# Kernel optimization log

Hardware: AMD Instinct MI355X
Metric: run time of the kernel (lower is better)

Reference implementation:

```python
import jax, jax.numpy as jnp
import numpy as np

N = 50000       # nodes
E = 1_600_000   # edges (before self-loops)
IN = 128        # in_channels
OUT = 32        # out_channels per head
H = 2           # heads
NEG_SLOPE = 0.2 # PyG GATConv default leaky-relu slope


def setup_inputs() -> dict:
    key = jax.random.key(0)
    k = jax.random.split(key, 6)
    x = jax.random.normal(k[0], (N, IN), jnp.float32)
    edge_index = jax.random.randint(k[1], (2, E), 0, N, dtype=jnp.int64)
    W = jax.random.normal(k[2], (IN, H * OUT), jnp.float32) / np.sqrt(IN).astype(np.float32)
    att_src = jax.random.normal(k[3], (H, OUT), jnp.float32) * 0.1
    att_dst = jax.random.normal(k[4], (H, OUT), jnp.float32) * 0.1
    bias = jax.random.normal(k[5], (H * OUT,), jnp.float32) * 0.01
    return {"x": x, "edge_index": edge_index, "W": W,
            "att_src": att_src, "att_dst": att_dst, "bias": bias}


def reference(x, edge_index, W, att_src, att_dst, bias):
    n = x.shape[0]
    h_, c = att_src.shape
    # add self-loops (PyG GATConv default add_self_loops=True)
    loops = jnp.arange(n, dtype=edge_index.dtype)
    src = jnp.concatenate([edge_index[0], loops])  # [E+N]
    dst = jnp.concatenate([edge_index[1], loops])  # [E+N]
    # linear transform -> [N, H, C]
    h = (x @ W).reshape(n, h_, c)
    # per-node attention logits per head
    a_src = jnp.einsum('nhc,hc->nh', h, att_src)  # [N, H]
    a_dst = jnp.einsum('nhc,hc->nh', h, att_dst)  # [N, H]
    # per-edge scores
    e = jax.nn.leaky_relu(a_src[src] + a_dst[dst], NEG_SLOPE)  # [E+N, H]
    # segment softmax over incoming edges of each dst node
    seg_max = jax.ops.segment_max(e, dst, num_segments=n)      # [N, H]
    ex = jnp.exp(e - seg_max[dst])
    denom = jax.ops.segment_sum(ex, dst, num_segments=n)       # [N, H]
    alpha = ex / denom[dst]                                    # [E+N, H]
    # weighted scatter-aggregate of source features
    msg = alpha[:, :, None] * h[src]                           # [E+N, H, C]
    out = jax.ops.segment_sum(msg, dst, num_segments=n)        # [N, H, C]
    return out.reshape(n, h_ * c) + bias
```

## Files before the change

kernel.cpp:

```cpp
#include <hip/hip_runtime.h>
#include <hip/hip_fp16.h>

#define N_NODES 50000
#define N_EDGES 1600000
#define IN_CH   128
#define NEG     0.2f
#define NBUK    391
#define BCAP    4608
#define CAP     80
#define CHUNK   4096
#define P_BLOCKS 391
#define PT      512

__global__ __launch_bounds__(256) void gemm_logits(
    const float* __restrict__ x, const float* __restrict__ W,
    const float* __restrict__ att_src, const float* __restrict__ att_dst,
    unsigned int* __restrict__ hI, float* __restrict__ as_, float* __restrict__ ad_,
    int* __restrict__ gcur)
{
    if (blockIdx.x == 0) {
        for (int i = threadIdx.x; i < NBUK; i += 256) gcur[i] = 0;
    }

    __shared__ float Wl[IN_CH * 64];
    for (int i = threadIdx.x; i < IN_CH * 64; i += 256) Wl[i] = W[i];
    __syncthreads();

    int gid = blockIdx.x * 256 + threadIdx.x;
    int row = gid >> 2;
    int sub = gid & 3;
    if (row >= N_NODES) return;

    float acc[16];
#pragma unroll
    for (int c = 0; c < 16; ++c) acc[c] = 0.f;

    const float* xr = x + (size_t)row * IN_CH;
    for (int k = 0; k < IN_CH; k += 4) {
        float4 xv = *(const float4*)(xr + k);
        float xs[4] = {xv.x, xv.y, xv.z, xv.w};
#pragma unroll
        for (int kk = 0; kk < 4; ++kk) {
            const float* wr = &Wl[(k + kk) * 64 + sub * 16];
#pragma unroll
            for (int c = 0; c < 16; c += 4) {
                float4 wv = *(const float4*)(wr + c);
                acc[c]     += xs[kk] * wv.x;
                acc[c + 1] += xs[kk] * wv.y;
                acc[c + 2] += xs[kk] * wv.z;
                acc[c + 3] += xs[kk] * wv.w;
            }
        }
    }

    float part[16];
#pragma unroll
    for (int i = 0; i < 16; ++i) part[i] = __shfl_xor(acc[i], 2);

    if (sub < 2) {
        union { unsigned int u[16]; uint4 v4[4]; } pk;
#pragma unroll
        for (int i = 0; i < 16; ++i) {
            pk.u[i] = (unsigned)__half_as_ushort(__float2half_rn(acc[i])) |
                      ((unsigned)__half_as_ushort(__float2half_rn(part[i])) << 16);
        }
        uint4* hp = (uint4*)(hI + (size_t)row * 32 + sub * 16);
#pragma unroll
        for (int i = 0; i < 4; ++i) hp[i] = pk.v4[i];
    }

    float s = 0.f, d = 0.f;
#pragma unroll
    for (int c = 0; c < 16; ++c) {
        s += acc[c] * att_src[sub * 16 + c];
        d += acc[c] * att_dst[sub * 16 + c];
    }
    s += __shfl_xor(s, 1);
    d += __shfl_xor(d, 1);
    if ((sub & 1) == 0) {
        as_[row * 2 + (sub >> 1)] = s;
        ad_[row * 2 + (sub >> 1)] = d;
    }
}

__global__ __launch_bounds__(PT) void partition(
    const int* __restrict__ ei, int* __restrict__ gcur,
    unsigned int* __restrict__ barr)
{
    __shared__ int hist[NBUK];
    __shared__ int start[NBUK];
    __shared__ int gbase[NBUK];
    __shared__ int lofs[NBUK];
    __shared__ int wsum[8];
    __shared__ int woff[8];
    __shared__ unsigned int buf[CHUNK];

    int tid = threadIdx.x;
    int lane = tid & 63, wid = tid >> 6;
    int cbase = blockIdx.x * CHUNK;
    int cnt = N_EDGES - cbase;
    if (cnt > CHUNK) cnt = CHUNK;
    int n4 = cnt >> 2;

    for (int i = tid; i < NBUK; i += PT) { hist[i] = 0; lofs[i] = 0; }
    __syncthreads();

    const int4* s4 = (const int4*)ei + (cbase >> 2);
    const int4* d4 = (const int4*)(ei + N_EDGES) + (cbase >> 2);

    int4 dv[2], sv[2];
#pragma unroll
    for (int i = 0; i < 2; ++i) {
        int k = i * PT + tid;
        if (k < n4) {
            dv[i] = d4[k]; sv[i] = s4[k];
            atomicAdd(&hist[dv[i].x >> 7], 1);
            atomicAdd(&hist[dv[i].y >> 7], 1);
            atomicAdd(&hist[dv[i].z >> 7], 1);
            atomicAdd(&hist[dv[i].w >> 7], 1);
        }
    }
    __syncthreads();

    int a = (tid < NBUK) ? hist[tid] : 0;
    int orig = a;
#pragma unroll
    for (int off = 1; off < 64; off <<= 1) {
        int u = __shfl_up(a, off);
        if (lane >= off) a += u;
    }
    if (lane == 63) wsum[wid] = a;
    __syncthreads();
    if (tid == 0) {
        int r = 0;
#pragma unroll
        for (int w = 0; w < 8; ++w) { woff[w] = r; r += wsum[w]; }
    }
    __syncthreads();
    a += woff[wid];
    if (tid < NBUK) {
        start[tid] = a - orig;
        gbase[tid] = atomicAdd(&gcur[tid], orig);
    }
    __syncthreads();

#pragma unroll
    for (int i = 0; i < 2; ++i) {
        int k = i * PT + tid;
        if (k < n4) {
            int dd[4] = {dv[i].x, dv[i].y, dv[i].z, dv[i].w};
            int ss[4] = {sv[i].x, sv[i].y, sv[i].z, sv[i].w};
#pragma unroll
            for (int e = 0; e < 4; ++e) {
                int d = dd[e];
                int bkt = d >> 7;
                int loc = atomicAdd(&lofs[bkt], 1);
                buf[start[bkt] + loc] =
                    (unsigned)ss[e] | ((unsigned)(d & 127) << 16) | ((unsigned)bkt << 23);
            }
        }
    }
    __syncthreads();

    for (int i = tid; i < cnt; i += PT) {
        unsigned u = buf[i];
        int bkt = u >> 23;
        int g = gbase[bkt] + (i - start[bkt]);
        if (g < BCAP) barr[(size_t)bkt * BCAP + g] = u & 0x7FFFFFu;
    }
}

__global__ __launch_bounds__(1024) void aggregate(
    const unsigned int* __restrict__ hI, const float* __restrict__ as_,
    const float* __restrict__ ad_, const int* __restrict__ gcur,
    const unsigned int* __restrict__ barr, const float* __restrict__ bias,
    float* __restrict__ out)
{
    __shared__ unsigned short lcol[128 * CAP];
    __shared__ int hist[128];
    __shared__ int lofs[128];
    __shared__ int wtot;

    int b = blockIdx.x, tid = threadIdx.x;
    if (tid < 128) { hist[tid] = 0; lofs[tid] = 0; }
    __syncthreads();

    int cnt = gcur[b];
    if (cnt > BCAP) cnt = BCAP;
    const unsigned int* bb = barr + (size_t)b * BCAP;

    for (int i = tid; i < cnt; i += 1024)
        atomicAdd(&hist[(bb[i] >> 16) & 127], 1);
    __syncthreads();

    for (int i = tid; i < cnt; i += 1024) {
        unsigned u = bb[i];
        int dl = (u >> 16) & 127;
        int k = atomicAdd(&lofs[dl], 1);
        if (k < CAP) lcol[dl * CAP + k] = (unsigned short)(u & 0xFFFFu);
    }
    __syncthreads();

    int lane = tid & 63;
    int wave = tid >> 6;
    int c    = lane & 31;
    int hv   = lane >> 5;
    int sl   = lane & 32;
    float bi0 = bias[c], bi1 = bias[32 + c];

    for (int pass = 0; pass < 4; ++pass) {
        int dl = pass * 32 + (wave << 1) + hv;
        int node = b * 128 + dl;
        bool valid = (node < N_NODES);

        float2 adv = valid ? *(const float2*)(ad_ + node * 2) : make_float2(0.f, 0.f);
        float2 asv = valid ? *(const float2*)(as_ + node * 2) : make_float2(0.f, 0.f);

        float t0 = asv.x + adv.x, t1 = asv.y + adv.y;
        float e0 = (t0 > 0.f) ? t0 : NEG * t0;
        float e1 = (t1 > 0.f) ? t1 : NEG * t1;
        float p0s = __expf(e0), p1s = __expf(e1);
        unsigned hs = valid ? hI[(unsigned)node * 32u + c] : 0u;
        float h0s = __half2float(__ushort_as_half((unsigned short)(hs & 0xFFFFu)));
        float h1s = __half2float(__ushort_as_half((unsigned short)(hs >> 16)));
        float acc0a = p0s * h0s, acc0b = 0.f;
        float acc1a = p1s * h1s, acc1b = 0.f;
        float s0 = 0.f, s1 = 0.f;

        int n = valid ? min(hist[dl], CAP) : 0;
        const unsigned short* cb = &lcol[dl * CAP];
        int nmax = max(n, __shfl_xor(n, 32));

        for (int base = 0; base < nmax; base += 32) {
            unsigned pack1 = 0, pack2 = 0;
            int myidx = base + c;
            if (myidx < n) {
                int msrc = (int)cb[myidx];
                float2 av = *(const float2*)(as_ + msrc * 2);
                float u0 = av.x + adv.x, u1 = av.y + adv.y;
                float f0 = (u0 > 0.f) ? u0 : NEG * u0;
                float f1 = (u1 > 0.f) ? u1 : NEG * u1;
                float q0 = __expf(f0), q1 = __expf(f1);
                s0 += q0; s1 += q1;
                pack1 = ((unsigned)msrc << 16) |
                        (unsigned)__half_as_ushort(__float2half_rn(q0));
                pack2 = (unsigned)__half_as_ushort(__float2half_rn(q1));
            }
            int c32 = nmax - base;
            if (c32 > 32) c32 = 32;

            int jj = 0;
            for (; jj + 4 <= c32; jj += 4) {
                unsigned aA = __shfl(pack1, sl + jj);
                unsigned bA = __shfl(pack2, sl + jj);
                unsigned aB = __shfl(pack1, sl + jj + 1);
                unsigned bB = __shfl(pack2, sl + jj + 1);
                unsigned aC = __shfl(pack1, sl + jj + 2);
                unsigned bC = __shfl(pack2, sl + jj + 2);
                unsigned aD = __shfl(pack1, sl + jj + 3);
                unsigned bD = __shfl(pack2, sl + jj + 3);
                unsigned vA = hI[(aA >> 16) * 32u + c];
                unsigned vB = hI[(aB >> 16) * 32u + c];
                unsigned vC = hI[(aC >> 16) * 32u + c];
                unsigned vD = hI[(aD >> 16) * 32u + c];
                float pA0 = __half2float(__ushort_as_half((unsigned short)aA));
                float pA1 = __half2float(__ushort_as_half((unsigned short)bA));
                float pB0 = __half2float(__ushort_as_half((unsigned short)aB));
                float pB1 = __half2float(__ushort_as_half((unsigned short)bB));
                float pC0 = __half2float(__ushort_as_half((unsigned short)aC));
                float pC1 = __half2float(__ushort_as_half((unsigned short)bC));
                float pD0 = __half2float(__ushort_as_half((unsigned short)aD));
                float pD1 = __half2float(__ushort_as_half((unsigned short)bD));
                acc0a = fmaf(pA0, __half2float(__ushort_as_half((unsigned short)(vA & 0xFFFFu))), acc0a);
                acc1a = fmaf(pA1, __half2float(__ushort_as_half((unsigned short)(vA >> 16))), acc1a);
                acc0b = fmaf(pB0, __half2float(__ushort_as_half((unsigned short)(vB & 0xFFFFu))), acc0b);
                acc1b = fmaf(pB1, __half2float(__ushort_as_half((unsigned short)(vB >> 16))), acc1b);
                acc0a = fmaf(pC0, __half2float(__ushort_as_half((unsigned short)(vC & 0xFFFFu))), acc0a);
                acc1a = fmaf(pC1, __half2float(__ushort_as_half((unsigned short)(vC >> 16))), acc1a);
                acc0b = fmaf(pD0, __half2float(__ushort_as_half((unsigned short)(vD & 0xFFFFu))), acc0b);
                acc1b = fmaf(pD1, __half2float(__ushort_as_half((unsigned short)(vD >> 16))), acc1b);
            }
            for (; jj < c32; ++jj) {
                unsigned aA = __shfl(pack1, sl + jj);
                unsigned bA = __shfl(pack2, sl + jj);
                unsigned vA = hI[(aA >> 16) * 32u + c];
                float pA0 = __half2float(__ushort_as_half((unsigned short)aA));
                float pA1 = __half2float(__ushort_as_half((unsigned short)bA));
                acc0a = fmaf(pA0, __half2float(__ushort_as_half((unsigned short)(vA & 0xFFFFu))), acc0a);
                acc1a = fmaf(pA1, __half2float(__ushort_as_half((unsigned short)(vA >> 16))), acc1a);
            }
        }

        s0 += __shfl_xor(s0, 16); s1 += __shfl_xor(s1, 16);
        s0 += __shfl_xor(s0, 8);  s1 += __shfl_xor(s1, 8);
        s0 += __shfl_xor(s0, 4);  s1 += __shfl_xor(s1, 4);
        s0 += __shfl_xor(s0, 2);  s1 += __shfl_xor(s1, 2);
        s0 += __shfl_xor(s0, 1);  s1 += __shfl_xor(s1, 1);
        s0 += p0s; s1 += p1s;

        if (valid) {
            out[(size_t)node * 64 + c]      = (acc0a + acc0b) / s0 + bi0;
            out[(size_t)node * 64 + 32 + c] = (acc1a + acc1b) / s1 + bi1;
        }
    }
}

extern "C" void kernel_launch(void* const* d_in, const int* in_sizes, int n_in,
                              void* d_out, int out_size, void* d_ws, size_t ws_size,
                              hipStream_t stream)
{
    const float* x       = (const float*)d_in[0];
    const int*   ei      = (const int*)d_in[1];
    const float* W       = (const float*)d_in[2];
    const float* att_src = (const float*)d_in[3];
    const float* att_dst = (const float*)d_in[4];
    const float* bias    = (const float*)d_in[5];
    float* out = (float*)d_out;

    char* ws = (char*)d_ws;
    size_t off = 0;
    auto alloc = [&](size_t bytes) -> void* {
        void* p = ws + off;
        off = (off + bytes + 511) & ~(size_t)511;
        return p;
    };
    unsigned int* hI  = (unsigned int*)alloc((size_t)N_NODES * 32 * 4);
    float*  as_ = (float*)alloc((size_t)N_NODES * 2 * 4);
    float*  ad_ = (float*)alloc((size_t)N_NODES * 2 * 4);
    int*    gcur = (int*)alloc((size_t)NBUK * 4);
    unsigned int* barr = (unsigned int*)alloc((size_t)NBUK * BCAP * 4);

    gemm_logits<<<(N_NODES * 4 + 255) / 256, 256, 0, stream>>>(
        x, W, att_src, att_dst, hI, as_, ad_, gcur);
    partition<<<P_BLOCKS, PT, 0, stream>>>(ei, gcur, barr);
    aggregate<<<NBUK, 1024, 0, stream>>>(hI, as_, ad_, gcur, barr, bias, out);
}
```

Measured before the change: 85.28 us.

## Split partition and aggregate work across twice as many smaller blocks

The partition kernel now processes 2048-edge chunks with 782 blocks, one int4 per thread, instead of 4096-edge chunks with 391 blocks. The aggregate kernel splits each 128-node bucket across two 512-thread blocks, each handling 64 destination rows. Each aggregate block makes a single pass over the bucket, counting and placing its own rows with one atomic and no separate histogram pass. The aim is more blocks in flight and better CU occupancy on a 256-CU part, at the cost of every bucket being read twice from global memory.

```diff
diff --git a/kernel.cpp b/kernel.cpp
--- a/kernel.cpp
+++ b/kernel.cpp
@@ -8,8 +8,8 @@
 #define NBUK    391
 #define BCAP    4608
 #define CAP     80
-#define CHUNK   4096
-#define P_BLOCKS 391
+#define CHUNK   2048
+#define P_BLOCKS 782
 #define PT      512
 
 __global__ __launch_bounds__(256) void gemm_logits(
@@ -108,17 +108,14 @@
     const int4* s4 = (const int4*)ei + (cbase >> 2);
     const int4* d4 = (const int4*)(ei + N_EDGES) + (cbase >> 2);
 
-    int4 dv[2], sv[2];
-#pragma unroll
-    for (int i = 0; i < 2; ++i) {
-        int k = i * PT + tid;
-        if (k < n4) {
-            dv[i] = d4[k]; sv[i] = s4[k];
-            atomicAdd(&hist[dv[i].x >> 7], 1);
-            atomicAdd(&hist[dv[i].y >> 7], 1);
-            atomicAdd(&hist[dv[i].z >> 7], 1);
-            atomicAdd(&hist[dv[i].w >> 7], 1);
-        }
+    int4 dv, sv;
+    bool have = (tid < n4);
+    if (have) {
+        dv = d4[tid]; sv = s4[tid];
+        atomicAdd(&hist[dv.x >> 7], 1);
+        atomicAdd(&hist[dv.y >> 7], 1);
+        atomicAdd(&hist[dv.z >> 7], 1);
+        atomicAdd(&hist[dv.w >> 7], 1);
     }
     __syncthreads();
 
@@ -144,20 +141,16 @@
     }
     __syncthreads();
 
-#pragma unroll
-    for (int i = 0; i < 2; ++i) {
-        int k = i * PT + tid;
-        if (k < n4) {
-            int dd[4] = {dv[i].x, dv[i].y, dv[i].z, dv[i].w};
-            int ss[4] = {sv[i].x, sv[i].y, sv[i].z, sv[i].w};
-#pragma unroll
-            for (int e = 0; e < 4; ++e) {
-                int d = dd[e];
-                int bkt = d >> 7;
-                int loc = atomicAdd(&lofs[bkt], 1);
-                buf[start[bkt] + loc] =
-                    (unsigned)ss[e] | ((unsigned)(d & 127) << 16) | ((unsigned)bkt << 23);
-            }
+    if (have) {
+        int dd[4] = {dv.x, dv.y, dv.z, dv.w};
+        int ss[4] = {sv.x, sv.y, sv.z, sv.w};
+#pragma unroll
+        for (int e = 0; e < 4; ++e) {
+            int d = dd[e];
+            int bkt = d >> 7;
+            int loc = atomicAdd(&lofs[bkt], 1);
+            buf[start[bkt] + loc] =
+                (unsigned)ss[e] | ((unsigned)(d & 127) << 16) | ((unsigned)bkt << 23);
         }
     }
     __syncthreads();
@@ -170,34 +163,32 @@
     }
 }
 
-__global__ __launch_bounds__(1024) void aggregate(
+__global__ __launch_bounds__(512) void aggregate(
     const unsigned int* __restrict__ hI, const float* __restrict__ as_,
     const float* __restrict__ ad_, const int* __restrict__ gcur,
     const unsigned int* __restrict__ barr, const float* __restrict__ bias,
     float* __restrict__ out)
 {
-    __shared__ unsigned short lcol[128 * CAP];
-    __shared__ int hist[128];
-    __shared__ int lofs[128];
-    __shared__ int wtot;
-
-    int b = blockIdx.x, tid = threadIdx.x;
-    if (tid < 128) { hist[tid] = 0; lofs[tid] = 0; }
+    __shared__ unsigned short lcol[64 * CAP];
+    __shared__ int hist[64];
+
+    int b    = blockIdx.x >> 1;
+    int jbase = (blockIdx.x & 1) << 6;
+    int tid  = threadIdx.x;
+    if (tid < 64) hist[tid] = 0;
     __syncthreads();
 
     int cnt = gcur[b];
     if (cnt > BCAP) cnt = BCAP;
     const unsigned int* bb = barr + (size_t)b * BCAP;
 
-    for (int i = tid; i < cnt; i += 1024)
-        atomicAdd(&hist[(bb[i] >> 16) & 127], 1);
-    __syncthreads();
-
-    for (int i = tid; i < cnt; i += 1024) {
+    for (int i = tid; i < cnt; i += 512) {
         unsigned u = bb[i];
-        int dl = (u >> 16) & 127;
-        int k = atomicAdd(&lofs[dl], 1);
-        if (k < CAP) lcol[dl * CAP + k] = (unsigned short)(u & 0xFFFFu);
+        int r = ((int)(u >> 16) & 127) - jbase;
+        if ((unsigned)r < 64u) {
+            int k = atomicAdd(&hist[r], 1);
+            if (k < CAP) lcol[r * CAP + k] = (unsigned short)(u & 0xFFFFu);
+        }
     }
     __syncthreads();
 
@@ -209,8 +200,8 @@
     float bi0 = bias[c], bi1 = bias[32 + c];
 
     for (int pass = 0; pass < 4; ++pass) {
-        int dl = pass * 32 + (wave << 1) + hv;
-        int node = b * 128 + dl;
+        int r = pass * 16 + (wave << 1) + hv;
+        int node = b * 128 + jbase + r;
         bool valid = (node < N_NODES);
 
         float2 adv = valid ? *(const float2*)(ad_ + node * 2) : make_float2(0.f, 0.f);
@@ -227,8 +218,8 @@
         float acc1a = p1s * h1s, acc1b = 0.f;
         float s0 = 0.f, s1 = 0.f;
 
-        int n = valid ? min(hist[dl], CAP) : 0;
-        const unsigned short* cb = &lcol[dl * CAP];
+        int n = valid ? min(hist[r], CAP) : 0;
+        const unsigned short* cb = &lcol[r * CAP];
         int nmax = max(n, __shfl_xor(n, 32));
 
         for (int base = 0; base < nmax; base += 32) {
@@ -333,5 +324,5 @@
     gemm_logits<<<(N_NODES * 4 + 255) / 256, 256, 0, stream>>>(
         x, W, att_src, att_dst, hI, as_, ad_, gcur);
     partition<<<P_BLOCKS, PT, 0, stream>>>(ei, gcur, barr);
-    aggregate<<<NBUK, 1024, 0, stream>>>(hI, as_, ad_, gcur, barr, bias, out);
+    aggregate<<<NBUK * 2, 512, 0, stream>>>(hI, as_, ad_, gcur, barr, bias, out);
 }
```

After: 91.56 us. 7.4% more time.
